# Optimization experiments

Hardware: AMD Instinct MI355X
Metric: run time of the kernel (lower is better)

Reference implementation:

```python
import jax, jax.numpy as jnp
import numpy as np

EPS = 1e-9


def _resolve(circle_pos, circle_radius, aabb_pos, aabb_half):
    Nc = circle_pos.shape[0]
    Na = aabb_pos.shape[0]

    # ---- circle vs circle: push apart along center-to-center normal ----
    d = circle_pos[:, None, :] - circle_pos[None, :, :]          # [Nc,Nc,2]
    d2 = jnp.sum(d * d, axis=-1)                                 # [Nc,Nc]
    off_diag = ~jnp.eye(Nc, dtype=bool)
    dist = jnp.sqrt(jnp.where(d2 > EPS, d2, 1.0))
    pen = circle_radius[:, None] + circle_radius[None, :] - dist
    hit = off_diag & (d2 > EPS) & (pen > 0)
    normal = d / dist[..., None]
    # each body moves half the penetration toward itself; summing over the
    # full (symmetric) matrix resolves every unordered pair exactly once
    corr_cc = jnp.sum(jnp.where(hit[..., None], 0.5 * pen[..., None] * normal, 0.0), axis=1)

    # ---- aabb vs aabb: push along minimum-overlap axis ----
    da = aabb_pos[:, None, :] - aabb_pos[None, :, :]             # [Na,Na,2]
    ov = aabb_half[:, None, :] + aabb_half[None, :, :] - jnp.abs(da)
    hit_a = (~jnp.eye(Na, dtype=bool)) & (ov[..., 0] > 0) & (ov[..., 1] > 0)
    sgn = jnp.where(da >= 0, 1.0, -1.0)
    use_x = ov[..., 0] <= ov[..., 1]
    zeros = jnp.zeros_like(ov[..., 0])
    push_x = jnp.stack([0.5 * ov[..., 0] * sgn[..., 0], zeros], axis=-1)
    push_y = jnp.stack([zeros, 0.5 * ov[..., 1] * sgn[..., 1]], axis=-1)
    push = jnp.where(use_x[..., None], push_x, push_y)
    corr_aa = jnp.sum(jnp.where(hit_a[..., None], push, 0.0), axis=1)

    # ---- circle vs aabb: closest point on box ----
    rel = circle_pos[:, None, :] - aabb_pos[None, :, :]          # [Nc,Na,2]
    closest = jnp.clip(rel, -aabb_half[None, :, :], aabb_half[None, :, :])
    diff = rel - closest
    dd2 = jnp.sum(diff * diff, axis=-1)
    ddist = jnp.sqrt(jnp.where(dd2 > EPS, dd2, 1.0))
    pen_ca = circle_radius[:, None] - ddist
    hit_ca = (dd2 > EPS) & (pen_ca > 0)
    n_ca = diff / ddist[..., None]
    push_ca = jnp.where(hit_ca[..., None], 0.5 * pen_ca[..., None] * n_ca, 0.0)
    corr_c = jnp.sum(push_ca, axis=1)     # on circles
    corr_a = -jnp.sum(push_ca, axis=0)    # equal-and-opposite on boxes

    new_circle = circle_pos + corr_cc + corr_c
    new_aabb = aabb_pos + corr_aa + corr_a
    return jnp.concatenate([new_circle, new_aabb], axis=0)   # [Nc+Na, 2]


def setup_inputs() -> dict:
    key = jax.random.key(0)
    k1, k2, k3, k4 = jax.random.split(key, 4)
    circle_pos = jax.random.normal(k1, (4096, 2), dtype=jnp.float32)
    circle_radius = jax.random.uniform(k2, (4096,), dtype=jnp.float32)
    aabb_pos = jax.random.normal(k3, (2048, 2), dtype=jnp.float32)
    aabb_half = jax.random.uniform(k4, (2048, 2), dtype=jnp.float32)
    return {"circle_pos": circle_pos, "circle_radius": circle_radius,
            "aabb_pos": aabb_pos, "aabb_half": aabb_half}


def reference(circle_pos, circle_radius, aabb_pos, aabb_half):
    return _resolve(circle_pos, circle_radius, aabb_pos, aabb_half)
```

## Files before the change

### kernel.cpp

```cpp
#include <hip/hip_runtime.h>
#include <math.h>

#define EPS 1e-9f

__device__ __forceinline__ int tri_off(int I) { return I * (193 - I) / 2; }

__global__ __launch_bounds__(256)
void collide(const float2* __restrict__ cpos,
             const float*  __restrict__ crad,
             const float2* __restrict__ apos,
             const float2* __restrict__ ahalf,
             float* __restrict__ out,
             int Nc) {
    const int lane = threadIdx.x & 63;
    const int w    = threadIdx.x >> 6;
    const int t    = blockIdx.x * 4 + w;

    int I = (int)((193.0f - sqrtf((float)(37249 - 8 * t))) * 0.5f);
    while (tri_off(I + 1) <= t) ++I;
    while (tri_off(I) > t) --I;
    const int J = I + (t - tri_off(I));

    const int tileC  = Nc >> 6;
    const bool bodyC = I < tileC;
    const bool partC = J < tileC;

    __shared__ float4 Jd[4][128];

    {
        const int j = (J << 6) + lane;
        float4 q;
        if (partC) {
            const float2 c = cpos[j];
            q = make_float4(c.x, c.y, 0.5f * crad[j], 0.0f);
        } else {
            const float2 a = apos[j - Nc];
            const float2 h = ahalf[j - Nc];
            q = make_float4(a.x, a.y, h.x, h.y);
        }
        Jd[w][lane]      = q;
        Jd[w][lane + 64] = q;
    }
    __syncthreads();

    const int i = (I << 6) + lane;
    float4 me;
    if (bodyC) {
        const float2 c = cpos[i];
        me = make_float4(c.x, c.y, 0.5f * crad[i], 0.0f);
    } else {
        const float2 a = apos[i - Nc];
        const float2 h = ahalf[i - Nc];
        me = make_float4(a.x, a.y, h.x, h.y);
    }

    float ax = 0.0f, ay = 0.0f;
    const int src = (lane + 1) & 63;

    if (I != J) {
        float gx = 0.0f, gy = 0.0f;
        if (partC) {
            const float px = me.x, py = me.y, rih = me.z;
            #pragma unroll 4
            for (int m = 0; m < 64; ++m) {
                const float4 q = Jd[w][lane + m];
                const float dx = q.x - px, dy = q.y - py;
                const float d2 = fmaf(dx, dx, dy * dy);
                const float r  = __builtin_amdgcn_rsqf(d2);
                const float s  = fmaxf(fmaf(rih + q.z, r, -0.5f), 0.0f);
                const float fx = s * dx, fy = s * dy;
                ax -= fx; ay -= fy;
                gx += fx; gy += fy;
                gx = __shfl(gx, src, 64);
                gy = __shfl(gy, src, 64);
            }
        } else if (bodyC) {
            const float px = me.x, py = me.y, rih = me.z;
            #pragma unroll 4
            for (int m = 0; m < 64; ++m) {
                const float4 q = Jd[w][lane + m];
                const float rx = q.x - px, ry = q.y - py;
                const float cx = fminf(fmaxf(rx, -q.z), q.z);
                const float cy = fminf(fmaxf(ry, -q.w), q.w);
                const float dx = rx - cx, dy = ry - cy;
                const float d2 = fmaf(dx, dx, dy * dy);
                const float r  = __builtin_amdgcn_rsqf(d2);
                float s = fmaxf(fmaf(rih, r, -0.5f), 0.0f);
                s = (d2 > EPS) ? s : 0.0f;
                const float fx = s * dx, fy = s * dy;
                ax -= fx; ay -= fy;
                gx += fx; gy += fy;
                gx = __shfl(gx, src, 64);
                gy = __shfl(gy, src, 64);
            }
        } else {
            const float bx = me.x, by = me.y, hx = me.z, hy = me.w;
            #pragma unroll 4
            for (int m = 0; m < 64; ++m) {
                const float4 q = Jd[w][lane + m];
                const float dqx = q.x - bx, dqy = q.y - by;
                const float ovx = (hx + q.z) - fabsf(dqx);
                const float ovy = (hy + q.w) - fabsf(dqy);
                const bool hit = fminf(ovx, ovy) > 0.0f;
                const bool ux  = ovx <= ovy;
                const float fx = (hit && ux)  ? copysignf(0.5f * ovx, dqx) : 0.0f;
                const float fy = (hit && !ux) ? copysignf(0.5f * ovy, dqy) : 0.0f;
                ax -= fx; ay -= fy;
                gx += fx; gy += fy;
                gx = __shfl(gx, src, 64);
                gy = __shfl(gy, src, 64);
            }
        }
        atomicAdd(&out[(((J << 6) + lane) << 1)],     gx);
        atomicAdd(&out[(((J << 6) + lane) << 1) + 1], gy);
    } else {
        if (bodyC) {
            const float px = me.x, py = me.y, rih = me.z;
            #pragma unroll 7
            for (int k = 1; k < 64; ++k) {
                const float4 q = Jd[w][lane + k];
                const float dx = px - q.x, dy = py - q.y;
                const float d2 = fmaf(dx, dx, dy * dy);
                const float r  = __builtin_amdgcn_rsqf(d2);
                const float s  = fmaxf(fmaf(rih + q.z, r, -0.5f), 0.0f);
                ax = fmaf(s, dx, ax); ay = fmaf(s, dy, ay);
            }
        } else {
            const float bx = me.x, by = me.y, hx = me.z, hy = me.w;
            #pragma unroll 7
            for (int k = 1; k < 64; ++k) {
                const float4 q = Jd[w][lane + k];
                const float dax = bx - q.x, day = by - q.y;
                const float ovx = (hx + q.z) - fabsf(dax);
                const float ovy = (hy + q.w) - fabsf(day);
                const bool hit = fminf(ovx, ovy) > 0.0f;
                const bool ux  = ovx <= ovy;
                ax += (hit && ux)  ? copysignf(0.5f * ovx, dax) : 0.0f;
                ay += (hit && !ux) ? copysignf(0.5f * ovy, day) : 0.0f;
            }
        }
        ax += me.x; ay += me.y;
    }

    atomicAdd(&out[(i << 1)],     ax);
    atomicAdd(&out[(i << 1) + 1], ay);
}

extern "C" void kernel_launch(void* const* d_in, const int* in_sizes, int n_in,
                              void* d_out, int out_size, void* d_ws, size_t ws_size,
                              hipStream_t stream) {
    (void)n_in; (void)d_ws; (void)ws_size;

    const float2* cpos  = (const float2*)d_in[0];
    const float*  crad  = (const float*) d_in[1];
    const float2* apos  = (const float2*)d_in[2];
    const float2* ahalf = (const float2*)d_in[3];

    const int Nc = in_sizes[1];

    hipMemsetAsync(d_out, 0, (size_t)out_size * sizeof(float), stream);

    const int tile_pairs = (96 * 97) / 2;
    const int blocks = tile_pairs / 4;
    collide<<<blocks, 256, 0, stream>>>(cpos, crad, apos, ahalf, (float*)d_out, Nc);
}
```

Measured before the change: 77.28 us.

## Replace atomic accumulation with per-tile workspace partials and a reduction kernel

Each tile-pair warp now writes its partial forces for both tiles into a dense 96x96x64 float2 workspace instead of doing float atomicAdds. A second kernel sums the 96 partials per body tile and writes the output directly, which also removes the memset. The aim is to avoid atomic contention. The cost is an extra launch and about 4.7MB of workspace traffic. The old atomic path is kept as a fallback when the workspace is too small.

```diff
diff --git a/kernel.cpp b/kernel.cpp
--- a/kernel.cpp
+++ b/kernel.cpp
@@ -6,12 +6,12 @@
 __device__ __forceinline__ int tri_off(int I) { return I * (193 - I) / 2; }
 
 __global__ __launch_bounds__(256)
-void collide(const float2* __restrict__ cpos,
-             const float*  __restrict__ crad,
-             const float2* __restrict__ apos,
-             const float2* __restrict__ ahalf,
-             float* __restrict__ out,
-             int Nc) {
+void collide_ws(const float2* __restrict__ cpos,
+                const float*  __restrict__ crad,
+                const float2* __restrict__ apos,
+                const float2* __restrict__ ahalf,
+                float2* __restrict__ ws,
+                int Nc) {
     const int lane = threadIdx.x & 63;
     const int w    = threadIdx.x >> 6;
     const int t    = blockIdx.x * 4 + w;
@@ -111,8 +111,7 @@
                 gy = __shfl(gy, src, 64);
             }
         }
-        atomicAdd(&out[(((J << 6) + lane) << 1)],     gx);
-        atomicAdd(&out[(((J << 6) + lane) << 1) + 1], gy);
+        ws[(J * 96 + I) * 64 + lane] = make_float2(gx, gy);
     } else {
         if (bodyC) {
             const float px = me.x, py = me.y, rih = me.z;
@@ -142,6 +141,160 @@
         ax += me.x; ay += me.y;
     }
 
+    ws[(I * 96 + J) * 64 + lane] = make_float2(ax, ay);
+}
+
+__global__ __launch_bounds__(64)
+void reduce_ws(const float2* __restrict__ ws, float2* __restrict__ out) {
+    const int T = blockIdx.x;
+    const int l = threadIdx.x;
+    const float2* row = ws + (size_t)(T * 96) * 64 + l;
+    float sx = 0.0f, sy = 0.0f;
+    #pragma unroll 8
+    for (int P = 0; P < 96; ++P) {
+        const float2 v = row[(size_t)P * 64];
+        sx += v.x; sy += v.y;
+    }
+    out[(T << 6) + l] = make_float2(sx, sy);
+}
+
+__global__ __launch_bounds__(256)
+void collide_atomic(const float2* __restrict__ cpos,
+                    const float*  __restrict__ crad,
+                    const float2* __restrict__ apos,
+                    const float2* __restrict__ ahalf,
+                    float* __restrict__ out,
+                    int Nc) {
+    const int lane = threadIdx.x & 63;
+    const int w    = threadIdx.x >> 6;
+    const int t    = blockIdx.x * 4 + w;
+
+    int I = (int)((193.0f - sqrtf((float)(37249 - 8 * t))) * 0.5f);
+    while (tri_off(I + 1) <= t) ++I;
+    while (tri_off(I) > t) --I;
+    const int J = I + (t - tri_off(I));
+
+    const int tileC  = Nc >> 6;
+    const bool bodyC = I < tileC;
+    const bool partC = J < tileC;
+
+    __shared__ float4 Jd[4][128];
+
+    {
+        const int j = (J << 6) + lane;
+        float4 q;
+        if (partC) {
+            const float2 c = cpos[j];
+            q = make_float4(c.x, c.y, 0.5f * crad[j], 0.0f);
+        } else {
+            const float2 a = apos[j - Nc];
+            const float2 h = ahalf[j - Nc];
+            q = make_float4(a.x, a.y, h.x, h.y);
+        }
+        Jd[w][lane]      = q;
+        Jd[w][lane + 64] = q;
+    }
+    __syncthreads();
+
+    const int i = (I << 6) + lane;
+    float4 me;
+    if (bodyC) {
+        const float2 c = cpos[i];
+        me = make_float4(c.x, c.y, 0.5f * crad[i], 0.0f);
+    } else {
+        const float2 a = apos[i - Nc];
+        const float2 h = ahalf[i - Nc];
+        me = make_float4(a.x, a.y, h.x, h.y);
+    }
+
+    float ax = 0.0f, ay = 0.0f;
+    const int src = (lane + 1) & 63;
+
+    if (I != J) {
+        float gx = 0.0f, gy = 0.0f;
+        if (partC) {
+            const float px = me.x, py = me.y, rih = me.z;
+            #pragma unroll 4
+            for (int m = 0; m < 64; ++m) {
+                const float4 q = Jd[w][lane + m];
+                const float dx = q.x - px, dy = q.y - py;
+                const float d2 = fmaf(dx, dx, dy * dy);
+                const float r  = __builtin_amdgcn_rsqf(d2);
+                const float s  = fmaxf(fmaf(rih + q.z, r, -0.5f), 0.0f);
+                const float fx = s * dx, fy = s * dy;
+                ax -= fx; ay -= fy;
+                gx += fx; gy += fy;
+                gx = __shfl(gx, src, 64);
+                gy = __shfl(gy, src, 64);
+            }
+        } else if (bodyC) {
+            const float px = me.x, py = me.y, rih = me.z;
+            #pragma unroll 4
+            for (int m = 0; m < 64; ++m) {
+                const float4 q = Jd[w][lane + m];
+                const float rx = q.x - px, ry = q.y - py;
+                const float cx = fminf(fmaxf(rx, -q.z), q.z);
+                const float cy = fminf(fmaxf(ry, -q.w), q.w);
+                const float dx = rx - cx, dy = ry - cy;
+                const float d2 = fmaf(dx, dx, dy * dy);
+                const float r  = __builtin_amdgcn_rsqf(d2);
+                float s = fmaxf(fmaf(rih, r, -0.5f), 0.0f);
+                s = (d2 > EPS) ? s : 0.0f;
+                const float fx = s * dx, fy = s * dy;
+                ax -= fx; ay -= fy;
+                gx += fx; gy += fy;
+                gx = __shfl(gx, src, 64);
+                gy = __shfl(gy, src, 64);
+            }
+        } else {
+            const float bx = me.x, by = me.y, hx = me.z, hy = me.w;
+            #pragma unroll 4
+            for (int m = 0; m < 64; ++m) {
+                const float4 q = Jd[w][lane + m];
+                const float dqx = q.x - bx, dqy = q.y - by;
+                const float ovx = (hx + q.z) - fabsf(dqx);
+                const float ovy = (hy + q.w) - fabsf(dqy);
+                const bool hit = fminf(ovx, ovy) > 0.0f;
+                const bool ux  = ovx <= ovy;
+                const float fx = (hit && ux)  ? copysignf(0.5f * ovx, dqx) : 0.0f;
+                const float fy = (hit && !ux) ? copysignf(0.5f * ovy, dqy) : 0.0f;
+                ax -= fx; ay -= fy;
+                gx += fx; gy += fy;
+                gx = __shfl(gx, src, 64);
+                gy = __shfl(gy, src, 64);
+            }
+        }
+        atomicAdd(&out[(((J << 6) + lane) << 1)],     gx);
+        atomicAdd(&out[(((J << 6) + lane) << 1) + 1], gy);
+    } else {
+        if (bodyC) {
+            const float px = me.x, py = me.y, rih = me.z;
+            #pragma unroll 7
+            for (int k = 1; k < 64; ++k) {
+                const float4 q = Jd[w][lane + k];
+                const float dx = px - q.x, dy = py - q.y;
+                const float d2 = fmaf(dx, dx, dy * dy);
+                const float r  = __builtin_amdgcn_rsqf(d2);
+                const float s  = fmaxf(fmaf(rih + q.z, r, -0.5f), 0.0f);
+                ax = fmaf(s, dx, ax); ay = fmaf(s, dy, ay);
+            }
+        } else {
+            const float bx = me.x, by = me.y, hx = me.z, hy = me.w;
+            #pragma unroll 7
+            for (int k = 1; k < 64; ++k) {
+                const float4 q = Jd[w][lane + k];
+                const float dax = bx - q.x, day = by - q.y;
+                const float ovx = (hx + q.z) - fabsf(dax);
+                const float ovy = (hy + q.w) - fabsf(day);
+                const bool hit = fminf(ovx, ovy) > 0.0f;
+                const bool ux  = ovx <= ovy;
+                ax += (hit && ux)  ? copysignf(0.5f * ovx, dax) : 0.0f;
+                ay += (hit && !ux) ? copysignf(0.5f * ovy, day) : 0.0f;
+            }
+        }
+        ax += me.x; ay += me.y;
+    }
+
     atomicAdd(&out[(i << 1)],     ax);
     atomicAdd(&out[(i << 1) + 1], ay);
 }
@@ -149,7 +302,7 @@
 extern "C" void kernel_launch(void* const* d_in, const int* in_sizes, int n_in,
                               void* d_out, int out_size, void* d_ws, size_t ws_size,
                               hipStream_t stream) {
-    (void)n_in; (void)d_ws; (void)ws_size;
+    (void)n_in;
 
     const float2* cpos  = (const float2*)d_in[0];
     const float*  crad  = (const float*) d_in[1];
@@ -158,9 +311,18 @@
 
     const int Nc = in_sizes[1];
 
-    hipMemsetAsync(d_out, 0, (size_t)out_size * sizeof(float), stream);
-
     const int tile_pairs = (96 * 97) / 2;
     const int blocks = tile_pairs / 4;
-    collide<<<blocks, 256, 0, stream>>>(cpos, crad, apos, ahalf, (float*)d_out, Nc);
+
+    const size_t ws_need = (size_t)96 * 96 * 64 * sizeof(float2);
+
+    if (d_ws != nullptr && ws_size >= ws_need) {
+        float2* ws = (float2*)d_ws;
+        collide_ws<<<blocks, 256, 0, stream>>>(cpos, crad, apos, ahalf, ws, Nc);
+        reduce_ws<<<96, 64, 0, stream>>>(ws, (float2*)d_out);
+    } else {
+        hipMemsetAsync(d_out, 0, (size_t)out_size * sizeof(float), stream);
+        collide_atomic<<<blocks, 256, 0, stream>>>(cpos, crad, apos, ahalf,
+                                                   (float*)d_out, Nc);
+    }
 }
```

Measured after the change: 78.22 us, median of 2. About the same (+1.2%).
